# Performance work log

Measured on AMD Instinct MI355X. Metric: run time of the kernel, lower is better.

The kernel has to match this reference:

```python
import jax, jax.numpy as jnp
import numpy as np

TOP_K = 2
NORM_TOPK_PROB = True


def setup_inputs() -> dict:
    key = jax.random.key(0)
    k1, k2 = jax.random.split(key)
    hidden_states = jax.random.normal(k1, (4, 4096, 2048), dtype=jnp.float32)
    # gate weight [n_routed_experts, hidden_size], kaiming-uniform-like scale
    weight = jax.random.normal(k2, (64, 2048), dtype=jnp.float32) * 0.02
    return {"hidden_states": hidden_states, "weight": weight}


def reference(hidden_states, weight):
    bsz, seq_len, h = hidden_states.shape
    x = hidden_states.reshape(-1, h)                      # [T, H]
    logits = jnp.einsum("th,eh->te", x, weight)           # [T, E]
    scores = jax.nn.softmax(logits, axis=-1)              # [T, E]
    topk_weight, topk_idx = jax.lax.top_k(scores, TOP_K)  # [T, K] each
    if TOP_K > 1 and NORM_TOPK_PROB:
        topk_weight = topk_weight / (topk_weight.sum(axis=-1, keepdims=True) + 1e-20)
    return (topk_idx.reshape(bsz, seq_len, -1), topk_weight.reshape(bsz, seq_len, -1))
```

## Files before the change

kernel.cpp:

```cpp
#include <hip/hip_runtime.h>
#include <math.h>

#define H    2048
#define NE   64
#define TOKB 64
#define KC   128
#define NCH  16
#define NBUF 4
#define TAU  4.0e-3f
#define NEGF (-3.0e38f)

typedef __bf16 bf16x8 __attribute__((ext_vector_type(8)));
typedef float  f32x16 __attribute__((ext_vector_type(16)));

#define MFMA(a, b, c) __builtin_amdgcn_mfma_f32_32x32x16_bf16((a), (b), (c), 0, 0, 0)
#define LD4(p) (*reinterpret_cast<const float4*>(p))

__device__ __forceinline__ void cvt8(const float4 a, const float4 b,
                                     bf16x8& hi, bf16x8& lo) {
    const float v0 = a.x, v1 = a.y, v2 = a.z, v3 = a.w;
    const float v4 = b.x, v5 = b.y, v6 = b.z, v7 = b.w;
    hi[0] = (__bf16)v0; lo[0] = (__bf16)(v0 - (float)hi[0]);
    hi[1] = (__bf16)v1; lo[1] = (__bf16)(v1 - (float)hi[1]);
    hi[2] = (__bf16)v2; lo[2] = (__bf16)(v2 - (float)hi[2]);
    hi[3] = (__bf16)v3; lo[3] = (__bf16)(v3 - (float)hi[3]);
    hi[4] = (__bf16)v4; lo[4] = (__bf16)(v4 - (float)hi[4]);
    hi[5] = (__bf16)v5; lo[5] = (__bf16)(v5 - (float)hi[5]);
    hi[6] = (__bf16)v6; lo[6] = (__bf16)(v6 - (float)hi[6]);
    hi[7] = (__bf16)v7; lo[7] = (__bf16)(v7 - (float)hi[7]);
}

__device__ __forceinline__ void gll16(const void* g, void* l) {
    __builtin_amdgcn_global_load_lds(
        (const __attribute__((address_space(1))) void*)g,
        (__attribute__((address_space(3))) void*)l, 16, 0, 0);
}

__global__ __launch_bounds__(256) void prep_w(
    const float* __restrict__ w, __bf16* __restrict__ wp, int* __restrict__ wl)
{
    const int e   = blockIdx.x;
    const int tid = threadIdx.x;
    if (e == 0 && tid == 0) wl[0] = 0;
    const float4 a = LD4(&w[e * H + tid * 8]);
    const float4 b = LD4(&w[e * H + tid * 8 + 4]);
    bf16x8 hi, lo;
    cvt8(a, b, hi, lo);
    const int g  = tid >> 1;
    const int kh = tid & 1;
    char* base = (char*)wp + (size_t)g * 4096 + kh * 1024 + e * 16;
    *reinterpret_cast<bf16x8*>(base)        = hi;
    *reinterpret_cast<bf16x8*>(base + 2048) = lo;
}

__global__ __launch_bounds__(512) void moe_gate_mfma(
    const float* __restrict__ x,
    const __bf16* __restrict__ wp,
    float* __restrict__ out, int woff,
    int* __restrict__ wl, int wlcap)
{
    extern __shared__ char lds[];

    const int tid  = threadIdx.x;
    const int lane = tid & 63;
    const int wv   = tid >> 6;
    const int mt   = wv >> 2;
    const int kq   = wv & 3;
    const int lo5  = lane & 31;
    const int hi5  = lane >> 5;
    const int t0   = blockIdx.x * TOKB;

    const char* sbase[4];
    #pragma unroll
    for (int q = 0; q < 4; ++q) {
        const int idx16 = q * 512 + tid;
        const int row   = idx16 >> 5;
        const int sl    = idx16 & 31;
        sbase[q] = (const char*)x + (size_t)(t0 + row) * 8192
                   + ((sl ^ (row & 31)) * 16);
    }

    f32x16 acc0, acc1;
    #pragma unroll
    for (int i = 0; i < 16; ++i) { acc0[i] = 0.f; acc1[i] = 0.f; }

    #pragma unroll
    for (int p = 0; p < 3; ++p)
        #pragma unroll
        for (int q = 0; q < 4; ++q)
            gll16(sbase[q] + p * 512, lds + p * 32768 + (q * 512 + wv * 64) * 16);

    const int rb  = mt * 32 + lo5;
    const int rbk = rb & 31;
    const int sb0 = kq * 8 + hi5 * 2;
    const int sb1 = kq * 8 + 4 + hi5 * 2;
    const int offB00 = rb * 512 + (((sb0)     ^ rbk) << 4);
    const int offB01 = rb * 512 + (((sb0 + 1) ^ rbk) << 4);
    const int offB10 = rb * 512 + (((sb1)     ^ rbk) << 4);
    const int offB11 = rb * 512 + (((sb1 + 1) ^ rbk) << 4);

    const char* wpb = (const char*)wp + hi5 * 1024 + lo5 * 16;

    for (int c = 0; c < NCH; ++c) {
        if (c < NCH - 2) {
            asm volatile("s_waitcnt vmcnt(8)" ::: "memory");
        } else if (c == NCH - 2) {
            asm volatile("s_waitcnt vmcnt(4)" ::: "memory");
        } else {
            asm volatile("s_waitcnt vmcnt(0)" ::: "memory");
        }
        __builtin_amdgcn_s_barrier();

        const char* wg = wpb + (size_t)(c * 8 + kq * 2) * 4096;
        const bf16x8 ah0a = *reinterpret_cast<const bf16x8*>(wg);
        const bf16x8 ah1a = *reinterpret_cast<const bf16x8*>(wg + 512);
        const bf16x8 al0a = *reinterpret_cast<const bf16x8*>(wg + 2048);
        const bf16x8 al1a = *reinterpret_cast<const bf16x8*>(wg + 2560);
        const bf16x8 ah0b = *reinterpret_cast<const bf16x8*>(wg + 4096);
        const bf16x8 ah1b = *reinterpret_cast<const bf16x8*>(wg + 4608);
        const bf16x8 al0b = *reinterpret_cast<const bf16x8*>(wg + 6144);
        const bf16x8 al1b = *reinterpret_cast<const bf16x8*>(wg + 6656);

        const char* bufb = lds + (c & 3) * 32768;
        const float4 b00 = *reinterpret_cast<const float4*>(bufb + offB00);
        const float4 b01 = *reinterpret_cast<const float4*>(bufb + offB01);
        const float4 b10 = *reinterpret_cast<const float4*>(bufb + offB10);
        const float4 b11 = *reinterpret_cast<const float4*>(bufb + offB11);

        if (c + 3 < NCH) {
            #pragma unroll
            for (int q = 0; q < 4; ++q)
                gll16(sbase[q] + (c + 3) * 512,
                      lds + ((c + 3) & 3) * 32768 + (q * 512 + wv * 64) * 16);
        }

        bf16x8 bh0, bl0, bh1, bl1;
        cvt8(b00, b01, bh0, bl0);
        cvt8(b10, b11, bh1, bl1);

        acc0 = MFMA(ah0a, bh0, acc0);
        acc1 = MFMA(ah1a, bh0, acc1);
        acc0 = MFMA(ah0a, bl0, acc0);
        acc1 = MFMA(ah1a, bl0, acc1);
        acc0 = MFMA(al0a, bh0, acc0);
        acc1 = MFMA(al1a, bh0, acc1);
        acc0 = MFMA(ah0b, bh1, acc0);
        acc1 = MFMA(ah1b, bh1, acc1);
        acc0 = MFMA(ah0b, bl1, acc0);
        acc1 = MFMA(ah1b, bl1, acc1);
        acc0 = MFMA(al0b, bh1, acc0);
        acc1 = MFMA(al1b, bh1, acc1);
    }

    __syncthreads();
    float* S = reinterpret_cast<float*>(lds);
    if (kq != 0) {
        const int base = ((mt * 3 + (kq - 1)) * 32 + lo5) * 65;
        #pragma unroll
        for (int r = 0; r < 16; ++r) {
            const int e0 = (r & 3) + 8 * (r >> 2) + 4 * hi5;
            S[base + e0]      = acc0[r];
            S[base + 32 + e0] = acc1[r];
        }
    }
    __syncthreads();
    if (kq != 0) return;
    #pragma unroll
    for (int q = 0; q < 3; ++q) {
        const int base = ((mt * 3 + q) * 32 + lo5) * 65;
        #pragma unroll
        for (int r = 0; r < 16; ++r) {
            const int e0 = (r & 3) + 8 * (r >> 2) + 4 * hi5;
            acc0[r] += S[base + e0];
            acc1[r] += S[base + 32 + e0];
        }
    }

    float m1 = NEGF, m2 = NEGF, m3 = NEGF;
    int   i1 = 0, i2 = 0;
    #pragma unroll
    for (int r = 0; r < 16; ++r) {
        const float v = acc0[r];
        const int   e = (r & 3) + 8 * (r >> 2) + 4 * hi5;
        if (v > m1)      { m3 = m2; m2 = m1; i2 = i1; m1 = v; i1 = e; }
        else if (v > m2) { m3 = m2; m2 = v; i2 = e; }
        else if (v > m3) { m3 = v; }
    }
    #pragma unroll
    for (int r = 0; r < 16; ++r) {
        const float v = acc1[r];
        const int   e = 32 + (r & 3) + 8 * (r >> 2) + 4 * hi5;
        if (v > m1)      { m3 = m2; m2 = m1; i2 = i1; m1 = v; i1 = e; }
        else if (v > m2) { m3 = m2; m2 = v; i2 = e; }
        else if (v > m3) { m3 = v; }
    }

    const float n1 = __shfl_xor(m1, 32), n2 = __shfl_xor(m2, 32), n3 = __shfl_xor(m3, 32);
    const int   j1 = __shfl_xor(i1, 32), j2 = __shfl_xor(i2, 32);

    float a1, a2, a3, b1, b2, b3; int ia1, ia2, ib1, ib2;
    const bool aF = (m1 > n1) || (m1 == n1 && i1 < j1);
    if (aF) { a1=m1; a2=m2; a3=m3; ia1=i1; ia2=i2; b1=n1; b2=n2; b3=n3; ib1=j1; ib2=j2; }
    else    { a1=n1; a2=n2; a3=n3; ia1=j1; ia2=j2; b1=m1; b2=m2; b3=m3; ib1=i1; ib2=i2; }

    const float o1 = a1; const int oi1 = ia1;
    float o2, o3; int oi2;
    const bool a2F = (a2 > b1) || (a2 == b1 && ia2 < ib1);
    if (a2F) { o2 = a2; oi2 = ia2; o3 = (a3 > b1) ? a3 : b1; }
    else     { o2 = b1; oi2 = ib1; o3 = (a2 > b2) ? a2 : b2; }

    if (hi5 == 0) {
        const int t = t0 + mt * 32 + lo5;
        const float r = expf(o2 - o1);
        const float s = 1.0f + r;
        out[2 * t + 0]        = (float)oi1;
        out[2 * t + 1]        = (float)oi2;
        out[woff + 2 * t + 0] = 1.0f / s;
        out[woff + 2 * t + 1] = r / s;
        if ((o1 - o2 < TAU) || (o2 - o3 < TAU)) {
            const int pos = atomicAdd(wl, 1);
            if (pos < wlcap) wl[1 + pos] = t;
        }
    }
}

__global__ __launch_bounds__(256) void moe_refine_fp64(
    const float* __restrict__ x, const float* __restrict__ w,
    float* __restrict__ out, int woff,
    const int* __restrict__ wl, int wlcap)
{
    __shared__ double Sd[3][NE];
    const int lane = threadIdx.x & 63;
    const int wv   = threadIdx.x >> 6;
    const int ks   = wv * 512;
    int cnt = wl[0];
    if (cnt > wlcap) cnt = wlcap;

    for (int i = blockIdx.x; i < cnt; i += gridDim.x) {
        const int t = wl[1 + i];

        const float4 xa = LD4(&x[(size_t)t * H + ks + lane * 4]);
        const float4 xb = LD4(&x[(size_t)t * H + ks + 256 + lane * 4]);
        const double x0 = xa.x, x1 = xa.y, x2 = xa.z, x3 = xa.w;
        const double x4 = xb.x, x5 = xb.y, x6 = xb.z, x7 = xb.w;

        double myacc = 0.0;
        #pragma unroll 4
        for (int e = 0; e < NE; ++e) {
            const float4 wa = LD4(&w[(size_t)e * H + ks + lane * 4]);
            const float4 wb = LD4(&w[(size_t)e * H + ks + 256 + lane * 4]);
            double sA = 0.0, sB = 0.0;
            sA = fma((double)wa.x, x0, sA); sA = fma((double)wa.y, x1, sA);
            sA = fma((double)wa.z, x2, sA); sA = fma((double)wa.w, x3, sA);
            sB = fma((double)wb.x, x4, sB); sB = fma((double)wb.y, x5, sB);
            sB = fma((double)wb.z, x6, sB); sB = fma((double)wb.w, x7, sB);
            double s = sA + sB;
            #pragma unroll
            for (int off = 1; off < 64; off <<= 1)
                s += __shfl_xor(s, off);
            if (lane == e) myacc = s;
        }

        if (wv > 0) Sd[wv - 1][lane] = myacc;
        __syncthreads();
        if (wv == 0) {
            const double acc = ((myacc + Sd[0][lane]) + Sd[1][lane]) + Sd[2][lane];

            double v = acc; int bi = lane;
            #pragma unroll
            for (int off = 32; off > 0; off >>= 1) {
                double ov = __shfl_xor(v, off);
                int    oi = __shfl_xor(bi, off);
                if (ov > v || (ov == v && oi < bi)) { v = ov; bi = oi; }
            }
            const double m1 = v; const int i1 = bi;

            double v2 = (lane == i1) ? -1.0e300 : acc; int b2 = lane;
            #pragma unroll
            for (int off = 32; off > 0; off >>= 1) {
                double ov = __shfl_xor(v2, off);
                int    oi = __shfl_xor(b2, off);
                if (ov > v2 || (ov == v2 && oi < b2)) { v2 = ov; b2 = oi; }
            }
            const double m2 = v2; const int i2 = b2;

            if (lane == 0) {
                const double r = exp(m2 - m1);
                const double s = 1.0 + r;
                out[2 * t + 0]        = (float)i1;
                out[2 * t + 1]        = (float)i2;
                out[woff + 2 * t + 0] = (float)(1.0 / s);
                out[woff + 2 * t + 1] = (float)(r / s);
            }
        }
        __syncthreads();
    }
}

extern "C" void kernel_launch(void* const* d_in, const int* in_sizes, int n_in,
                              void* d_out, int out_size, void* d_ws, size_t ws_size,
                              hipStream_t stream) {
    const float* x   = (const float*)d_in[0];
    const float* wgt = (const float*)d_in[1];
    float* out = (float*)d_out;

    const int T    = in_sizes[0] / H;
    const int woff = out_size / 2;

    int*    wl = (int*)d_ws;
    __bf16* wp = (__bf16*)((char*)d_ws + 131072);
    int wlcap = T;

    (void)hipFuncSetAttribute((const void*)moe_gate_mfma,
                              hipFuncAttributeMaxDynamicSharedMemorySize, 131072);

    prep_w<<<dim3(NE), dim3(256), 0, stream>>>(wgt, wp, wl);

    moe_gate_mfma<<<dim3(T / TOKB), dim3(512), 131072, stream>>>(
        x, wp, out, woff, wl, wlcap);

    moe_refine_fp64<<<dim3(512), dim3(256), 0, stream>>>(
        x, wgt, out, woff, wl, wlcap);
}
```

Before: 67.58 us.

## Halve token tile to 32, split K across eight waves, prefetch weights

```diff
diff --git a/kernel.cpp b/kernel.cpp
--- a/kernel.cpp
+++ b/kernel.cpp
@@ -3,10 +3,9 @@
 
 #define H    2048
 #define NE   64
-#define TOKB 64
+#define TOKB 32
 #define KC   128
 #define NCH  16
-#define NBUF 4
 #define TAU  4.0e-3f
 #define NEGF (-3.0e38f)
 
@@ -54,8 +53,7 @@
 }
 
 __global__ __launch_bounds__(512) void moe_gate_mfma(
-    const float* __restrict__ x,
-    const __bf16* __restrict__ wp,
+    const float* __restrict__ x, const __bf16* __restrict__ wp,
     float* __restrict__ out, int woff,
     int* __restrict__ wl, int wlcap)
 {
@@ -63,99 +61,83 @@
 
     const int tid  = threadIdx.x;
     const int lane = tid & 63;
-    const int wv   = tid >> 6;
-    const int mt   = wv >> 2;
-    const int kq   = wv & 3;
+    const int kq   = tid >> 6;
     const int lo5  = lane & 31;
     const int hi5  = lane >> 5;
     const int t0   = blockIdx.x * TOKB;
 
-    const char* sbase[4];
-    #pragma unroll
-    for (int q = 0; q < 4; ++q) {
-        const int idx16 = q * 512 + tid;
-        const int row   = idx16 >> 5;
-        const int sl    = idx16 & 31;
-        sbase[q] = (const char*)x + (size_t)(t0 + row) * 8192
-                   + ((sl ^ (row & 31)) * 16);
-    }
+    const char* xb = (const char*)x;
+    const int u0 = tid, u1 = 512 + tid;
+    const int r0 = u0 >> 5, r1 = u1 >> 5;
+    const size_t xs0 = (size_t)(t0 + r0) * 8192 + (((u0 & 31) ^ r0) << 4);
+    const size_t xs1 = (size_t)(t0 + r1) * 8192 + (((u1 & 31) ^ (r1 & 31)) << 4);
+    const int ld0 = u0 * 16, ld1 = u1 * 16;
+
+    const char* wpA = (const char*)wp + kq * 4096 + hi5 * 1024 + lo5 * 16;
+
+    const int s0 = kq * 4 + hi5 * 2;
+    const int offB0 = lo5 * 512 + (((s0)     ^ lo5) << 4);
+    const int offB1 = lo5 * 512 + (((s0 + 1) ^ lo5) << 4);
 
     f32x16 acc0, acc1;
     #pragma unroll
     for (int i = 0; i < 16; ++i) { acc0[i] = 0.f; acc1[i] = 0.f; }
 
-    #pragma unroll
-    for (int p = 0; p < 3; ++p)
-        #pragma unroll
-        for (int q = 0; q < 4; ++q)
-            gll16(sbase[q] + p * 512, lds + p * 32768 + (q * 512 + wv * 64) * 16);
-
-    const int rb  = mt * 32 + lo5;
-    const int rbk = rb & 31;
-    const int sb0 = kq * 8 + hi5 * 2;
-    const int sb1 = kq * 8 + 4 + hi5 * 2;
-    const int offB00 = rb * 512 + (((sb0)     ^ rbk) << 4);
-    const int offB01 = rb * 512 + (((sb0 + 1) ^ rbk) << 4);
-    const int offB10 = rb * 512 + (((sb1)     ^ rbk) << 4);
-    const int offB11 = rb * 512 + (((sb1 + 1) ^ rbk) << 4);
-
-    const char* wpb = (const char*)wp + hi5 * 1024 + lo5 * 16;
-
+    bf16x8 A[2][4];
+
+    A[0][0] = *reinterpret_cast<const bf16x8*>(wpA);
+    A[0][1] = *reinterpret_cast<const bf16x8*>(wpA + 512);
+    A[0][2] = *reinterpret_cast<const bf16x8*>(wpA + 2048);
+    A[0][3] = *reinterpret_cast<const bf16x8*>(wpA + 2560);
+    __builtin_amdgcn_sched_barrier(0);
+    gll16(xb + xs0,        lds + 0 * 16384 + ld0);
+    gll16(xb + xs1,        lds + 0 * 16384 + ld1);
+    gll16(xb + xs0 + 512,  lds + 1 * 16384 + ld0);
+    gll16(xb + xs1 + 512,  lds + 1 * 16384 + ld1);
+    gll16(xb + xs0 + 1024, lds + 2 * 16384 + ld0);
+    gll16(xb + xs1 + 1024, lds + 2 * 16384 + ld1);
+    __builtin_amdgcn_sched_barrier(0);
+
+    #pragma unroll
     for (int c = 0; c < NCH; ++c) {
-        if (c < NCH - 2) {
-            asm volatile("s_waitcnt vmcnt(8)" ::: "memory");
-        } else if (c == NCH - 2) {
-            asm volatile("s_waitcnt vmcnt(4)" ::: "memory");
-        } else {
-            asm volatile("s_waitcnt vmcnt(0)" ::: "memory");
-        }
+        if (c == 0)       { asm volatile("s_waitcnt vmcnt(4)" ::: "memory"); }
+        else if (c <= 13) { asm volatile("s_waitcnt vmcnt(2)" ::: "memory"); }
+        else              { asm volatile("s_waitcnt vmcnt(0)" ::: "memory"); }
         __builtin_amdgcn_s_barrier();
 
-        const char* wg = wpb + (size_t)(c * 8 + kq * 2) * 4096;
-        const bf16x8 ah0a = *reinterpret_cast<const bf16x8*>(wg);
-        const bf16x8 ah1a = *reinterpret_cast<const bf16x8*>(wg + 512);
-        const bf16x8 al0a = *reinterpret_cast<const bf16x8*>(wg + 2048);
-        const bf16x8 al1a = *reinterpret_cast<const bf16x8*>(wg + 2560);
-        const bf16x8 ah0b = *reinterpret_cast<const bf16x8*>(wg + 4096);
-        const bf16x8 ah1b = *reinterpret_cast<const bf16x8*>(wg + 4608);
-        const bf16x8 al0b = *reinterpret_cast<const bf16x8*>(wg + 6144);
-        const bf16x8 al1b = *reinterpret_cast<const bf16x8*>(wg + 6656);
-
-        const char* bufb = lds + (c & 3) * 32768;
-        const float4 b00 = *reinterpret_cast<const float4*>(bufb + offB00);
-        const float4 b01 = *reinterpret_cast<const float4*>(bufb + offB01);
-        const float4 b10 = *reinterpret_cast<const float4*>(bufb + offB10);
-        const float4 b11 = *reinterpret_cast<const float4*>(bufb + offB11);
-
+        if (c + 1 < NCH) {
+            const char* wc = wpA + (size_t)(c + 1) * 32768;
+            A[(c + 1) & 1][0] = *reinterpret_cast<const bf16x8*>(wc);
+            A[(c + 1) & 1][1] = *reinterpret_cast<const bf16x8*>(wc + 512);
+            A[(c + 1) & 1][2] = *reinterpret_cast<const bf16x8*>(wc + 2048);
+            A[(c + 1) & 1][3] = *reinterpret_cast<const bf16x8*>(wc + 2560);
+        }
+        __builtin_amdgcn_sched_barrier(0);
         if (c + 3 < NCH) {
-            #pragma unroll
-            for (int q = 0; q < 4; ++q)
-                gll16(sbase[q] + (c + 3) * 512,
-                      lds + ((c + 3) & 3) * 32768 + (q * 512 + wv * 64) * 16);
-        }
-
-        bf16x8 bh0, bl0, bh1, bl1;
-        cvt8(b00, b01, bh0, bl0);
-        cvt8(b10, b11, bh1, bl1);
-
-        acc0 = MFMA(ah0a, bh0, acc0);
-        acc1 = MFMA(ah1a, bh0, acc1);
-        acc0 = MFMA(ah0a, bl0, acc0);
-        acc1 = MFMA(ah1a, bl0, acc1);
-        acc0 = MFMA(al0a, bh0, acc0);
-        acc1 = MFMA(al1a, bh0, acc1);
-        acc0 = MFMA(ah0b, bh1, acc0);
-        acc1 = MFMA(ah1b, bh1, acc1);
-        acc0 = MFMA(ah0b, bl1, acc0);
-        acc1 = MFMA(ah1b, bl1, acc1);
-        acc0 = MFMA(al0b, bh1, acc0);
-        acc1 = MFMA(al1b, bh1, acc1);
+            gll16(xb + xs0 + (size_t)(c + 3) * 512,
+                  lds + ((c + 3) & 3) * 16384 + ld0);
+            gll16(xb + xs1 + (size_t)(c + 3) * 512,
+                  lds + ((c + 3) & 3) * 16384 + ld1);
+        }
+        __builtin_amdgcn_sched_barrier(0);
+
+        const char* xbuf = lds + (c & 3) * 16384;
+        const float4 b1 = *reinterpret_cast<const float4*>(xbuf + offB0);
+        const float4 b2 = *reinterpret_cast<const float4*>(xbuf + offB1);
+        bf16x8 bh, bl;
+        cvt8(b1, b2, bh, bl);
+        acc0 = MFMA(A[c & 1][0], bh, acc0);
+        acc1 = MFMA(A[c & 1][1], bh, acc1);
+        acc0 = MFMA(A[c & 1][0], bl, acc0);
+        acc1 = MFMA(A[c & 1][1], bl, acc1);
+        acc0 = MFMA(A[c & 1][2], bh, acc0);
+        acc1 = MFMA(A[c & 1][3], bh, acc1);
     }
 
     __syncthreads();
     float* S = reinterpret_cast<float*>(lds);
     if (kq != 0) {
-        const int base = ((mt * 3 + (kq - 1)) * 32 + lo5) * 65;
+        const int base = ((kq - 1) * 32 + lo5) * 65;
         #pragma unroll
         for (int r = 0; r < 16; ++r) {
             const int e0 = (r & 3) + 8 * (r >> 2) + 4 * hi5;
@@ -166,8 +148,8 @@
     __syncthreads();
     if (kq != 0) return;
     #pragma unroll
-    for (int q = 0; q < 3; ++q) {
-        const int base = ((mt * 3 + q) * 32 + lo5) * 65;
+    for (int q = 1; q < 8; ++q) {
+        const int base = ((q - 1) * 32 + lo5) * 65;
         #pragma unroll
         for (int r = 0; r < 16; ++r) {
             const int e0 = (r & 3) + 8 * (r >> 2) + 4 * hi5;
@@ -210,7 +192,7 @@
     else     { o2 = b1; oi2 = ib1; o3 = (a2 > b2) ? a2 : b2; }
 
     if (hi5 == 0) {
-        const int t = t0 + mt * 32 + lo5;
+        const int t = t0 + lo5;
         const float r = expf(o2 - o1);
         const float s = 1.0f + r;
         out[2 * t + 0]        = (float)oi1;
@@ -312,11 +294,11 @@
     int wlcap = T;
 
     (void)hipFuncSetAttribute((const void*)moe_gate_mfma,
-                              hipFuncAttributeMaxDynamicSharedMemorySize, 131072);
+                              hipFuncAttributeMaxDynamicSharedMemorySize, 65536);
 
     prep_w<<<dim3(NE), dim3(256), 0, stream>>>(wgt, wp, wl);
 
-    moe_gate_mfma<<<dim3(T / TOKB), dim3(512), 131072, stream>>>(
+    moe_gate_mfma<<<dim3(T / TOKB), dim3(512), 65536, stream>>>(
         x, wp, out, woff, wl, wlcap);
 
     moe_refine_fp64<<<dim3(512), dim3(256), 0, stream>>>(
```

Result: slower. 81.91 us (+21.2%).
